# Kernel tuning notes

Hardware: AMD Instinct MI355X
Metric: run time of the kernel (lower is better)

## Reference

```python
import jax, jax.numpy as jnp
import numpy as np


def setup_inputs() -> dict:
    key = jax.random.key(0)
    k1, k2, k3 = jax.random.split(key, 3)
    B, N, F, U = 8, 2048, 128, 128
    A = jax.random.uniform(k1, (B, N, N), dtype=jnp.float32)   # dense nonneg adjacency
    X = jax.random.normal(k2, (B, N, F), dtype=jnp.float32)
    W = jax.random.normal(k3, (F, U), dtype=jnp.float32)
    bias = jnp.zeros((U,), dtype=jnp.float32)
    p = jnp.zeros((1,), dtype=jnp.float32)
    q = jnp.zeros((1,), dtype=jnp.float32)
    return {"A": A, "X": X, "W": W, "bias": bias, "p": p, "q": q}


def reference(A, X, W, bias, p, q):
    # learn_pqr path of MyGCN: A_ = D @ (A + q*I) @ D with D = diag(k^-0.25),
    # k = p + (1-p)*colsum(A). Diag matmuls expressed as broadcasted scaling (same math).
    B, N, _ = A.shape
    ps = jax.nn.sigmoid(p)          # shape (1,)
    qs = jax.nn.sigmoid(q)
    Dr = jnp.sum(A, axis=1)          # [B, N]  (K.sum axis=1)
    k_vec = ps + (1.0 - ps) * Dr     # [B, N]
    k_inv_root = jnp.sqrt(k_vec) ** -0.5   # k^{-0.25}
    k_clean = jnp.where(jnp.isinf(k_inv_root), 0.0, k_inv_root)  # [B, N]
    I = jnp.eye(N, dtype=A.dtype)
    AqI = A + qs[0] * I              # [B, N, N]
    A_ = k_clean[:, :, None] * AqI * k_clean[:, None, :]
    XW = jnp.einsum('bnf,fu->bnu', X, W)        # [B, N, U]
    A_XW = jnp.einsum('bnm,bmu->bnu', A_, XW)   # [B, N, U]
    out = A_XW + bias
    return jax.nn.relu(out)
```

## Files before the change

### kernel.cpp

```cpp
#include <hip/hip_runtime.h>
#include <stdint.h>

#define N 2048
#define F 128
#define UDIM 128

typedef __attribute__((ext_vector_type(8))) __bf16 bf16x8;
typedef __attribute__((ext_vector_type(8))) unsigned short us8;
typedef __attribute__((ext_vector_type(4))) float f32x4;

__device__ __forceinline__ unsigned short f2bf(float f) {
  union { float f; uint32_t u; } v; v.f = f;
  uint32_t u = v.u;
  return (unsigned short)((u + 0x7FFFu + ((u >> 16) & 1u)) >> 16);
}
__device__ __forceinline__ float bf2f(unsigned short u) {
  union { uint32_t u; float f; } v; v.u = ((uint32_t)u) << 16; return v.f;
}

__device__ __forceinline__ void async_load16(const void* g, void* l) {
  typedef const __attribute__((address_space(1))) uint32_t* gp_t;
  typedef __attribute__((address_space(3))) uint32_t* lp_t;
  __builtin_amdgcn_global_load_lds((gp_t)(uintptr_t)g, (lp_t)(uint32_t)(uintptr_t)l, 16, 0, 0);
}

__global__ __launch_bounds__(256)
void gcn_colsum(const float* __restrict__ A, const float* __restrict__ W,
                float* __restrict__ partial, unsigned short* __restrict__ WTb) {
  const int b = blockIdx.z;
  const int rc = blockIdx.y;
  const int j = blockIdx.x * 1024 + threadIdx.x * 4;
  const float* ap = A + (size_t)b * N * N + (size_t)rc * 32 * N + j;
  float s0 = 0.f, s1 = 0.f, s2 = 0.f, s3 = 0.f;
  #pragma unroll 4
  for (int rr = 0; rr < 32; ++rr) {
    float4 v = *(const float4*)(ap + (size_t)rr * N);
    s0 += v.x; s1 += v.y; s2 += v.z; s3 += v.w;
  }
  float4 s; s.x = s0; s.y = s1; s.z = s2; s.w = s3;
  *(float4*)&partial[((size_t)b * 64 + rc) * N + j] = s;

  if (blockIdx.y == 0 && blockIdx.z == 0) {
    #pragma unroll 4
    for (int it = 0; it < 32; ++it) {
      const int flat = it * 512 + blockIdx.x * 256 + threadIdx.x;
      const int k_ = flat >> 7;
      const int u = flat & 127;
      WTb[u * 128 + k_] = f2bf(W[flat]);
    }
  }
}

__global__ __launch_bounds__(256, 2)
void gcn_xwT(const float* __restrict__ X, const unsigned short* __restrict__ WTb,
             const float* __restrict__ partial, const float* __restrict__ pptr,
             float* __restrict__ kcl, unsigned short* __restrict__ YT) {
  __shared__ __align__(16) unsigned short Wl[128 * 128];
  __shared__ __align__(16) unsigned short Xl[32 * 128];
  __shared__ float red[8][33];
  __shared__ float kct[32];

  const int t = threadIdx.x;
  const int lane = t & 63;
  const int wid = t >> 6;
  const int b = blockIdx.x >> 6;
  const int i0 = (blockIdx.x & 63) << 5;

  #pragma unroll
  for (int rnd = 0; rnd < 8; ++rnd) {
    const int u = rnd * 16 + (t >> 4);
    const int c16 = (t & 15) ^ (u & 7);
    async_load16(WTb + u * 128 + c16 * 8, &Wl[rnd * 2048 + (t & ~63) * 8]);
  }
  {
    const int r = t >> 3;
    const float* xp = X + ((size_t)b * N + i0 + r) * F + (t & 7) * 8;
    #pragma unroll
    for (int h = 0; h < 2; ++h) {
      float4 v0 = *(const float4*)(xp + h * 64);
      float4 v1 = *(const float4*)(xp + h * 64 + 4);
      us8 w;
      w[0] = f2bf(v0.x); w[1] = f2bf(v0.y); w[2] = f2bf(v0.z); w[3] = f2bf(v0.w);
      w[4] = f2bf(v1.x); w[5] = f2bf(v1.y); w[6] = f2bf(v1.z); w[7] = f2bf(v1.w);
      const int slot = (t & 7) + h * 8;
      *(us8*)&Xl[r * 128 + ((slot ^ (r & 7)) * 8)] = w;
    }
  }
  {
    const int col = t & 31;
    const int grp = t >> 5;
    float s = 0.f;
    #pragma unroll
    for (int rr = 0; rr < 8; ++rr)
      s += partial[((size_t)b * 64 + grp * 8 + rr) * N + i0 + col];
    red[grp][col] = s;
  }
  __syncthreads();
  if (t < 32) {
    float s = 0.f;
    #pragma unroll
    for (int g = 0; g < 8; ++g) s += red[g][t];
    const float sp = 1.0f / (1.0f + __expf(-pptr[0]));
    const float k = sp + (1.0f - sp) * s;
    float rv = rsqrtf(sqrtf(k));
    if (isinf(rv)) rv = 0.f;
    kct[t] = rv;
    kcl[b * N + i0 + t] = rv;
  }
  __syncthreads();

  f32x4 acc[2][2];
  #pragma unroll
  for (int a = 0; a < 2; ++a)
    #pragma unroll
    for (int c = 0; c < 2; ++c) { f32x4 z = {0.f, 0.f, 0.f, 0.f}; acc[a][c] = z; }

  const int u0 = wid * 32;
  #pragma unroll
  for (int kc = 0; kc < 4; ++kc) {
    bf16x8 af[2], bfv[2];
    #pragma unroll
    for (int ut = 0; ut < 2; ++ut) {
      const int u = u0 + ut * 16 + (lane & 15);
      const int sl = ((kc * 4 + (lane >> 4)) ^ (u & 7)) * 8;
      af[ut] = *(const bf16x8*)&Wl[u * 128 + sl];
    }
    #pragma unroll
    for (int it = 0; it < 2; ++it) {
      const int rr = it * 16 + (lane & 15);
      const int sl = ((kc * 4 + (lane >> 4)) ^ (rr & 7)) * 8;
      bfv[it] = *(const bf16x8*)&Xl[rr * 128 + sl];
    }
    #pragma unroll
    for (int ut = 0; ut < 2; ++ut)
      #pragma unroll
      for (int it = 0; it < 2; ++it)
        acc[ut][it] = __builtin_amdgcn_mfma_f32_16x16x32_bf16(af[ut], bfv[it], acc[ut][it], 0, 0, 0);
  }

  #pragma unroll
  for (int ut = 0; ut < 2; ++ut) {
    #pragma unroll
    for (int it = 0; it < 2; ++it) {
      const int ic = it * 16 + (lane & 15);
      const float kv = kct[ic];
      #pragma unroll
      for (int rg = 0; rg < 4; ++rg) {
        const int u = u0 + ut * 16 + (lane >> 4) * 4 + rg;
        YT[(size_t)b * UDIM * N + (size_t)u * N + i0 + ic] = f2bf(acc[ut][it][rg] * kv);
      }
    }
  }
}

__global__ __launch_bounds__(256, 2)
void gcn_gemm(const float* __restrict__ A, const unsigned short* __restrict__ YT,
              const float* __restrict__ kcl, const float* __restrict__ bias,
              const float* __restrict__ qptr, float* __restrict__ out) {
  __shared__ __align__(16) unsigned short Abuf[3][32 * 64];
  __shared__ __align__(16) unsigned short Ybuf[3][128 * 64];

  const int t = threadIdx.x;
  const int lane = t & 63;
  const int wid = t >> 6;
  const int wr = wid >> 1;
  const int wc = wid & 1;

  const int bid = blockIdx.x;
  const int b = bid & 7;
  const int i0 = (bid >> 3) << 5;

  const float qs = 1.0f / (1.0f + __expf(-qptr[0]));

  const int r = t >> 3;
  const int c8 = t & 7;
  const float* Ap = A + (size_t)b * N * N + (size_t)(i0 + r) * N + c8 * 8;
  const unsigned short* YTb = YT + (size_t)b * UDIM * N;

  const int a_woff = r * 64 + ((c8 ^ (r & 7)) * 8);
  const int y_u = t >> 3;
  const int y_wavebase = (t & ~63) * 8;

  f32x4 acc[4];
  #pragma unroll
  for (int i = 0; i < 4; ++i) { f32x4 z = {0.f, 0.f, 0.f, 0.f}; acc[i] = z; }

  float4 ar0, ar1;

  auto issueA = [&](int kt) {
    ar0 = *(const float4*)(Ap + kt * 64);
    ar1 = *(const float4*)(Ap + kt * 64 + 4);
  };
  auto issueY = [&](int kt, int buf) {
    const int k0 = kt * 64;
    #pragma unroll
    for (int rnd = 0; rnd < 4; ++rnd) {
      const int u = rnd * 32 + y_u;
      const int c16 = (t & 7) ^ (u & 7);
      async_load16(YTb + (size_t)u * N + k0 + c16 * 8, &Ybuf[buf][rnd * 2048 + y_wavebase]);
    }
  };
  auto convertA = [&](int buf) {
    us8 w;
    w[0] = f2bf(ar0.x); w[1] = f2bf(ar0.y); w[2] = f2bf(ar0.z); w[3] = f2bf(ar0.w);
    w[4] = f2bf(ar1.x); w[5] = f2bf(ar1.y); w[6] = f2bf(ar1.z); w[7] = f2bf(ar1.w);
    *(us8*)&Abuf[buf][a_woff] = w;
  };
  auto compute = [&](int cur) {
    #pragma unroll
    for (int kk = 0; kk < 2; ++kk) {
      const int ar = 16 * wr + (lane & 15);
      const int as = ((kk * 4 + (lane >> 4)) ^ (ar & 7)) * 8;
      bf16x8 af = *(const bf16x8*)&Abuf[cur][ar * 64 + as];
      #pragma unroll
      for (int ut = 0; ut < 4; ++ut) {
        const int u = 64 * wc + ut * 16 + (lane & 15);
        const int bs = ((kk * 4 + (lane >> 4)) ^ (u & 7)) * 8;
        bf16x8 bfv = *(const bf16x8*)&Ybuf[cur][u * 64 + bs];
        acc[ut] = __builtin_amdgcn_mfma_f32_16x16x32_bf16(af, bfv, acc[ut], 0, 0, 0);
      }
    }
  };

#define STEP(KT, CUR, NXT, ISS)                                  \
  {                                                              \
    asm volatile("s_waitcnt vmcnt(4)" ::: "memory");             \
    convertA(NXT);                                               \
    asm volatile("s_waitcnt lgkmcnt(0)" ::: "memory");           \
    __builtin_amdgcn_s_barrier();                                \
    __builtin_amdgcn_sched_barrier(0);                           \
    issueA((KT) + 2);                                            \
    __builtin_amdgcn_sched_barrier(0);                           \
    issueY((KT) + 2, (ISS));                                     \
    __builtin_amdgcn_sched_barrier(0);                           \
    compute(CUR);                                                \
  }

  issueA(0);
  __builtin_amdgcn_sched_barrier(0);
  issueY(0, 0);
  __builtin_amdgcn_sched_barrier(0);
  asm volatile("s_waitcnt vmcnt(4)" ::: "memory");
  convertA(0);
  __builtin_amdgcn_sched_barrier(0);
  issueA(1);
  __builtin_amdgcn_sched_barrier(0);
  issueY(1, 1);
  __builtin_amdgcn_sched_barrier(0);

  #pragma unroll 1
  for (int kt0 = 0; kt0 < 30; kt0 += 3) {
    STEP(kt0,     0, 1, 2);
    STEP(kt0 + 1, 1, 2, 0);
    STEP(kt0 + 2, 2, 0, 1);
  }
#undef STEP

  asm volatile("s_waitcnt vmcnt(4)" ::: "memory");
  convertA(1);
  asm volatile("s_waitcnt lgkmcnt(0)" ::: "memory");
  __builtin_amdgcn_s_barrier();
  __builtin_amdgcn_sched_barrier(0);
  compute(0);
  asm volatile("s_waitcnt vmcnt(0)" ::: "memory");
  __builtin_amdgcn_s_barrier();
  __builtin_amdgcn_sched_barrier(0);
  compute(1);

  const int irow = i0 + 16 * wr + (lane >> 4) * 4;
  #pragma unroll
  for (int ut = 0; ut < 4; ++ut) {
    const int u = 64 * wc + ut * 16 + (lane & 15);
    const float bv = bias[u];
    #pragma unroll
    for (int rg = 0; rg < 4; ++rg) {
      const int i = irow + rg;
      const float yv = bf2f(YTb[(size_t)u * N + i]);
      const float kv = kcl[b * N + i];
      float vv = kv * (acc[ut][rg] + qs * yv) + bv;
      out[((size_t)b * N + i) * UDIM + u] = vv > 0.f ? vv : 0.f;
    }
  }
}

extern "C" void kernel_launch(void* const* d_in, const int* in_sizes, int n_in,
                              void* d_out, int out_size, void* d_ws, size_t ws_size,
                              hipStream_t stream) {
  (void)in_sizes; (void)n_in; (void)out_size; (void)ws_size;
  const float* A    = (const float*)d_in[0];
  const float* X    = (const float*)d_in[1];
  const float* W    = (const float*)d_in[2];
  const float* bias = (const float*)d_in[3];
  const float* p    = (const float*)d_in[4];
  const float* q    = (const float*)d_in[5];
  float* out = (float*)d_out;

  char* ws = (char*)d_ws;
  float* partial      = (float*)ws;
  float* kcl          = (float*)(ws + 4194304);
  unsigned short* WTb = (unsigned short*)(ws + 4194304 + 65536);
  unsigned short* YT  = (unsigned short*)(ws + 4292608);

  gcn_colsum<<<dim3(2, 64, 8), dim3(256), 0, stream>>>(A, W, partial, WTb);
  gcn_xwT<<<dim3(512), dim3(256), 0, stream>>>(X, WTb, partial, p, kcl, YT);
  gcn_gemm<<<dim3(512), dim3(256), 0, stream>>>(A, YT, kcl, bias, q, out);
}
```

Measured before the change: 62.15 us.

## Merge colsum with XW GEMM, add scale pass, deepen main GEMM pipeline

```diff
diff --git a/kernel.cpp b/kernel.cpp
--- a/kernel.cpp
+++ b/kernel.cpp
@@ -17,6 +17,11 @@
 __device__ __forceinline__ float bf2f(unsigned short u) {
   union { uint32_t u; float f; } v; v.u = ((uint32_t)u) << 16; return v.f;
 }
+__device__ __forceinline__ uint32_t cvtpk(float lo, float hi) {
+  uint32_t r;
+  asm("v_cvt_pk_bf16_f32 %0, %1, %2" : "=v"(r) : "v"(lo), "v"(hi));
+  return r;
+}
 
 __device__ __forceinline__ void async_load16(const void* g, void* l) {
   typedef const __attribute__((address_space(1))) uint32_t* gp_t;
@@ -24,53 +29,53 @@
   __builtin_amdgcn_global_load_lds((gp_t)(uintptr_t)g, (lp_t)(uint32_t)(uintptr_t)l, 16, 0, 0);
 }
 
-__global__ __launch_bounds__(256)
-void gcn_colsum(const float* __restrict__ A, const float* __restrict__ W,
-                float* __restrict__ partial, unsigned short* __restrict__ WTb) {
-  const int b = blockIdx.z;
-  const int rc = blockIdx.y;
-  const int j = blockIdx.x * 1024 + threadIdx.x * 4;
-  const float* ap = A + (size_t)b * N * N + (size_t)rc * 32 * N + j;
-  float s0 = 0.f, s1 = 0.f, s2 = 0.f, s3 = 0.f;
-  #pragma unroll 4
-  for (int rr = 0; rr < 32; ++rr) {
-    float4 v = *(const float4*)(ap + (size_t)rr * N);
-    s0 += v.x; s1 += v.y; s2 += v.z; s3 += v.w;
-  }
-  float4 s; s.x = s0; s.y = s1; s.z = s2; s.w = s3;
-  *(float4*)&partial[((size_t)b * 64 + rc) * N + j] = s;
-
-  if (blockIdx.y == 0 && blockIdx.z == 0) {
-    #pragma unroll 4
-    for (int it = 0; it < 32; ++it) {
-      const int flat = it * 512 + blockIdx.x * 256 + threadIdx.x;
-      const int k_ = flat >> 7;
-      const int u = flat & 127;
-      WTb[u * 128 + k_] = f2bf(W[flat]);
-    }
-  }
-}
-
-__global__ __launch_bounds__(256, 2)
-void gcn_xwT(const float* __restrict__ X, const unsigned short* __restrict__ WTb,
-             const float* __restrict__ partial, const float* __restrict__ pptr,
-             float* __restrict__ kcl, unsigned short* __restrict__ YT) {
+__global__ __launch_bounds__(256, 4)
+void gcn_pass1(const float* __restrict__ A, const float* __restrict__ X,
+               const float* __restrict__ W, float* __restrict__ partial,
+               unsigned short* __restrict__ Z) {
   __shared__ __align__(16) unsigned short Wl[128 * 128];
   __shared__ __align__(16) unsigned short Xl[32 * 128];
-  __shared__ float red[8][33];
-  __shared__ float kct[32];
-
+
+  const int bid = blockIdx.x;
   const int t = threadIdx.x;
+
+  if (bid < 1024) {
+    const int b = bid >> 7;
+    const int rc = (bid >> 1) & 63;
+    const int j = (bid & 1) * 1024 + t * 4;
+    const float* ap = A + (size_t)b * N * N + (size_t)rc * 32 * N + j;
+    float s0 = 0.f, s1 = 0.f, s2 = 0.f, s3 = 0.f;
+    #pragma unroll 4
+    for (int rr = 0; rr < 32; ++rr) {
+      float4 v = *(const float4*)(ap + (size_t)rr * N);
+      s0 += v.x; s1 += v.y; s2 += v.z; s3 += v.w;
+    }
+    float4 s; s.x = s0; s.y = s1; s.z = s2; s.w = s3;
+    *(float4*)&partial[((size_t)b * 64 + rc) * N + j] = s;
+    return;
+  }
+
+  const int zid = bid - 1024;
   const int lane = t & 63;
   const int wid = t >> 6;
-  const int b = blockIdx.x >> 6;
-  const int i0 = (blockIdx.x & 63) << 5;
-
-  #pragma unroll
-  for (int rnd = 0; rnd < 8; ++rnd) {
-    const int u = rnd * 16 + (t >> 4);
-    const int c16 = (t & 15) ^ (u & 7);
-    async_load16(WTb + u * 128 + c16 * 8, &Wl[rnd * 2048 + (t & ~63) * 8]);
+  const int b = zid >> 6;
+  const int i0 = (zid & 63) << 5;
+
+  {
+    const int u = t & 127;
+    const int khalf = t >> 7;
+    #pragma unroll
+    for (int g = 0; g < 8; ++g) {
+      const int k0 = khalf * 64 + g * 8;
+      float v[8];
+      #pragma unroll
+      for (int e = 0; e < 8; ++e) v[e] = W[(size_t)(k0 + e) * 128 + u];
+      uint4 w;
+      w.x = cvtpk(v[0], v[1]); w.y = cvtpk(v[2], v[3]);
+      w.z = cvtpk(v[4], v[5]); w.w = cvtpk(v[6], v[7]);
+      const int slot = khalf * 8 + g;
+      *(uint4*)&Wl[u * 128 + ((slot ^ (u & 7)) * 8)] = w;
+    }
   }
   {
     const int r = t >> 3;
@@ -79,77 +84,101 @@
     for (int h = 0; h < 2; ++h) {
       float4 v0 = *(const float4*)(xp + h * 64);
       float4 v1 = *(const float4*)(xp + h * 64 + 4);
-      us8 w;
-      w[0] = f2bf(v0.x); w[1] = f2bf(v0.y); w[2] = f2bf(v0.z); w[3] = f2bf(v0.w);
-      w[4] = f2bf(v1.x); w[5] = f2bf(v1.y); w[6] = f2bf(v1.z); w[7] = f2bf(v1.w);
+      uint4 w;
+      w.x = cvtpk(v0.x, v0.y); w.y = cvtpk(v0.z, v0.w);
+      w.z = cvtpk(v1.x, v1.y); w.w = cvtpk(v1.z, v1.w);
       const int slot = (t & 7) + h * 8;
-      *(us8*)&Xl[r * 128 + ((slot ^ (r & 7)) * 8)] = w;
-    }
-  }
+      *(uint4*)&Xl[r * 128 + ((slot ^ (r & 7)) * 8)] = w;
+    }
+  }
+  __syncthreads();
+
+  f32x4 acc[2][2];
+  #pragma unroll
+  for (int a = 0; a < 2; ++a)
+    #pragma unroll
+    for (int c = 0; c < 2; ++c) { f32x4 z = {0.f, 0.f, 0.f, 0.f}; acc[a][c] = z; }
+
+  const int u0 = wid * 32;
+  #pragma unroll
+  for (int kc = 0; kc < 4; ++kc) {
+    bf16x8 af[2], bfv[2];
+    #pragma unroll
+    for (int ut = 0; ut < 2; ++ut) {
+      const int u = u0 + ut * 16 + (lane & 15);
+      const int sl = ((kc * 4 + (lane >> 4)) ^ (u & 7)) * 8;
+      af[ut] = *(const bf16x8*)&Wl[u * 128 + sl];
+    }
+    #pragma unroll
+    for (int it = 0; it < 2; ++it) {
+      const int rr = it * 16 + (lane & 15);
+      const int sl = ((kc * 4 + (lane >> 4)) ^ (rr & 7)) * 8;
+      bfv[it] = *(const bf16x8*)&Xl[rr * 128 + sl];
+    }
+    #pragma unroll
+    for (int ut = 0; ut < 2; ++ut)
+      #pragma unroll
+      for (int it = 0; it < 2; ++it)
+        acc[ut][it] = __builtin_amdgcn_mfma_f32_16x16x32_bf16(af[ut], bfv[it], acc[ut][it], 0, 0, 0);
+  }
+
+  #pragma unroll
+  for (int ut = 0; ut < 2; ++ut)
+    #pragma unroll
+    for (int it = 0; it < 2; ++it) {
+      const int ic = i0 + it * 16 + (lane & 15);
+      #pragma unroll
+      for (int rg = 0; rg < 4; ++rg) {
+        const int u = u0 + ut * 16 + (lane >> 4) * 4 + rg;
+        Z[((size_t)b * UDIM + u) * N + ic] = f2bf(acc[ut][it][rg]);
+      }
+    }
+}
+
+__global__ __launch_bounds__(256, 4)
+void gcn_scale(const float* __restrict__ partial, const float* __restrict__ pptr,
+               const unsigned short* __restrict__ Z, float* __restrict__ kcl,
+               unsigned short* __restrict__ YT) {
+  __shared__ float red[2][128];
+  __shared__ float kct[128];
+  const int t = threadIdx.x;
+  const int b = blockIdx.x >> 4;
+  const int ic = (blockIdx.x & 15) * 128;
+
   {
-    const int col = t & 31;
-    const int grp = t >> 5;
+    const int i = ic + (t & 127);
+    const int half = t >> 7;
     float s = 0.f;
-    #pragma unroll
-    for (int rr = 0; rr < 8; ++rr)
-      s += partial[((size_t)b * 64 + grp * 8 + rr) * N + i0 + col];
-    red[grp][col] = s;
+    #pragma unroll 8
+    for (int rc = half * 32; rc < half * 32 + 32; ++rc)
+      s += partial[((size_t)b * 64 + rc) * N + i];
+    red[half][t & 127] = s;
   }
   __syncthreads();
-  if (t < 32) {
-    float s = 0.f;
-    #pragma unroll
-    for (int g = 0; g < 8; ++g) s += red[g][t];
+  if (t < 128) {
+    const float s = red[0][t] + red[1][t];
     const float sp = 1.0f / (1.0f + __expf(-pptr[0]));
     const float k = sp + (1.0f - sp) * s;
     float rv = rsqrtf(sqrtf(k));
     if (isinf(rv)) rv = 0.f;
     kct[t] = rv;
-    kcl[b * N + i0 + t] = rv;
+    kcl[b * N + ic + t] = rv;
   }
   __syncthreads();
 
-  f32x4 acc[2][2];
-  #pragma unroll
-  for (int a = 0; a < 2; ++a)
-    #pragma unroll
-    for (int c = 0; c < 2; ++c) { f32x4 z = {0.f, 0.f, 0.f, 0.f}; acc[a][c] = z; }
-
-  const int u0 = wid * 32;
-  #pragma unroll
-  for (int kc = 0; kc < 4; ++kc) {
-    bf16x8 af[2], bfv[2];
-    #pragma unroll
-    for (int ut = 0; ut < 2; ++ut) {
-      const int u = u0 + ut * 16 + (lane & 15);
-      const int sl = ((kc * 4 + (lane >> 4)) ^ (u & 7)) * 8;
-      af[ut] = *(const bf16x8*)&Wl[u * 128 + sl];
-    }
-    #pragma unroll
-    for (int it = 0; it < 2; ++it) {
-      const int rr = it * 16 + (lane & 15);
-      const int sl = ((kc * 4 + (lane >> 4)) ^ (rr & 7)) * 8;
-      bfv[it] = *(const bf16x8*)&Xl[rr * 128 + sl];
-    }
-    #pragma unroll
-    for (int ut = 0; ut < 2; ++ut)
-      #pragma unroll
-      for (int it = 0; it < 2; ++it)
-        acc[ut][it] = __builtin_amdgcn_mfma_f32_16x16x32_bf16(af[ut], bfv[it], acc[ut][it], 0, 0, 0);
-  }
-
-  #pragma unroll
-  for (int ut = 0; ut < 2; ++ut) {
-    #pragma unroll
-    for (int it = 0; it < 2; ++it) {
-      const int ic = it * 16 + (lane & 15);
-      const float kv = kct[ic];
-      #pragma unroll
-      for (int rg = 0; rg < 4; ++rg) {
-        const int u = u0 + ut * 16 + (lane >> 4) * 4 + rg;
-        YT[(size_t)b * UDIM * N + (size_t)u * N + i0 + ic] = f2bf(acc[ut][it][rg] * kv);
-      }
-    }
+  const int i8 = (t & 15) * 8;
+  #pragma unroll
+  for (int it = 0; it < 8; ++it) {
+    const int u = it * 16 + (t >> 4);
+    const size_t off = ((size_t)b * UDIM + u) * N + ic + i8;
+    us8 z = *(const us8*)&Z[off];
+    float y[8];
+    #pragma unroll
+    for (int e = 0; e < 8; ++e) y[e] = bf2f(z[e]) * kct[i8 + e];
+    uint4 w;
+    w.x = cvtpk(y[0], y[1]); w.y = cvtpk(y[2], y[3]);
+    w.z = cvtpk(y[4], y[5]); w.w = cvtpk(y[6], y[7]);
+    *(uint4*)&YT[off] = w;
   }
 }
 
@@ -157,8 +186,8 @@
 void gcn_gemm(const float* __restrict__ A, const unsigned short* __restrict__ YT,
               const float* __restrict__ kcl, const float* __restrict__ bias,
               const float* __restrict__ qptr, float* __restrict__ out) {
-  __shared__ __align__(16) unsigned short Abuf[3][32 * 64];
-  __shared__ __align__(16) unsigned short Ybuf[3][128 * 64];
+  __shared__ __align__(16) unsigned short Abuf[4 * 32 * 64];
+  __shared__ __align__(16) unsigned short Ybuf[4 * 128 * 64];
 
   const int t = threadIdx.x;
   const int lane = t & 63;
@@ -185,87 +214,84 @@
   #pragma unroll
   for (int i = 0; i < 4; ++i) { f32x4 z = {0.f, 0.f, 0.f, 0.f}; acc[i] = z; }
 
-  float4 ar0, ar1;
-
-  auto issueA = [&](int kt) {
-    ar0 = *(const float4*)(Ap + kt * 64);
-    ar1 = *(const float4*)(Ap + kt * 64 + 4);
-  };
+  float4 a0A, a1A, a0B, a1B;
+
   auto issueY = [&](int kt, int buf) {
     const int k0 = kt * 64;
     #pragma unroll
     for (int rnd = 0; rnd < 4; ++rnd) {
       const int u = rnd * 32 + y_u;
       const int c16 = (t & 7) ^ (u & 7);
-      async_load16(YTb + (size_t)u * N + k0 + c16 * 8, &Ybuf[buf][rnd * 2048 + y_wavebase]);
-    }
-  };
-  auto convertA = [&](int buf) {
-    us8 w;
-    w[0] = f2bf(ar0.x); w[1] = f2bf(ar0.y); w[2] = f2bf(ar0.z); w[3] = f2bf(ar0.w);
-    w[4] = f2bf(ar1.x); w[5] = f2bf(ar1.y); w[6] = f2bf(ar1.z); w[7] = f2bf(ar1.w);
-    *(us8*)&Abuf[buf][a_woff] = w;
+      async_load16(YTb + (size_t)u * N + k0 + c16 * 8, &Ybuf[buf * 8192 + rnd * 2048 + y_wavebase]);
+    }
   };
   auto compute = [&](int cur) {
+    const unsigned short* Ac = Abuf + cur * 2048;
+    const unsigned short* Yc = Ybuf + cur * 8192;
     #pragma unroll
     for (int kk = 0; kk < 2; ++kk) {
       const int ar = 16 * wr + (lane & 15);
       const int as = ((kk * 4 + (lane >> 4)) ^ (ar & 7)) * 8;
-      bf16x8 af = *(const bf16x8*)&Abuf[cur][ar * 64 + as];
+      bf16x8 af = *(const bf16x8*)&Ac[ar * 64 + as];
       #pragma unroll
       for (int ut = 0; ut < 4; ++ut) {
         const int u = 64 * wc + ut * 16 + (lane & 15);
         const int bs = ((kk * 4 + (lane >> 4)) ^ (u & 7)) * 8;
-        bf16x8 bfv = *(const bf16x8*)&Ybuf[cur][u * 64 + bs];
+        bf16x8 bfv = *(const bf16x8*)&Yc[u * 64 + bs];
         acc[ut] = __builtin_amdgcn_mfma_f32_16x16x32_bf16(af, bfv, acc[ut], 0, 0, 0);
       }
     }
   };
 
-#define STEP(KT, CUR, NXT, ISS)                                  \
-  {                                                              \
-    asm volatile("s_waitcnt vmcnt(4)" ::: "memory");             \
-    convertA(NXT);                                               \
-    asm volatile("s_waitcnt lgkmcnt(0)" ::: "memory");           \
-    __builtin_amdgcn_s_barrier();                                \
-    __builtin_amdgcn_sched_barrier(0);                           \
-    issueA((KT) + 2);                                            \
-    __builtin_amdgcn_sched_barrier(0);                           \
-    issueY((KT) + 2, (ISS));                                     \
-    __builtin_amdgcn_sched_barrier(0);                           \
-    compute(CUR);                                                \
-  }
-
-  issueA(0);
-  __builtin_amdgcn_sched_barrier(0);
-  issueY(0, 0);
-  __builtin_amdgcn_sched_barrier(0);
+#define SB __builtin_amdgcn_sched_barrier(0)
+#define ISSUE_A(KT, R0, R1) { R0 = *(const float4*)(Ap + (KT) * 64); R1 = *(const float4*)(Ap + (KT) * 64 + 4); }
+#define CVT_A(BUF, R0, R1) { \
+    uint4 w; w.x = cvtpk(R0.x, R0.y); w.y = cvtpk(R0.z, R0.w); \
+    w.z = cvtpk(R1.x, R1.y); w.w = cvtpk(R1.z, R1.w); \
+    *(uint4*)&Abuf[(BUF) * 2048 + a_woff] = w; }
+
+  ISSUE_A(0, a0A, a1A); SB;
+  ISSUE_A(1, a0B, a1B); SB;
+  issueY(0, 0); SB;
+  asm volatile("s_waitcnt vmcnt(6)" ::: "memory");
+  CVT_A(0, a0A, a1A); SB;
+  ISSUE_A(2, a0A, a1A); SB;
+  issueY(1, 1); SB;
+  asm volatile("s_waitcnt vmcnt(10)" ::: "memory");
+  CVT_A(1, a0B, a1B); SB;
+  ISSUE_A(3, a0B, a1B); SB;
+  issueY(2, 2); SB;
+
+#define GSTEP(KT, VM, R0, R1, DO_A, DO_Y)                          \
+  {                                                                \
+    asm volatile("s_waitcnt vmcnt(" #VM ")" ::: "memory");         \
+    CVT_A(((KT) + 2) & 3, R0, R1);                                 \
+    asm volatile("s_waitcnt lgkmcnt(0)" ::: "memory");             \
+    __builtin_amdgcn_s_barrier(); SB;                              \
+    if (DO_A) { ISSUE_A((KT) + 4, R0, R1); } SB;                   \
+    if (DO_Y) { issueY((KT) + 3, ((KT) + 3) & 3); } SB;            \
+    __builtin_amdgcn_s_setprio(1);                                 \
+    compute((KT) & 3);                                             \
+    __builtin_amdgcn_s_setprio(0); SB;                             \
+  }
+
+  #pragma unroll 1
+  for (int kt = 0; kt < 28; kt += 2) {
+    GSTEP(kt, 10, a0A, a1A, true, true);
+    GSTEP(kt + 1, 10, a0B, a1B, true, true);
+  }
+  GSTEP(28, 10, a0A, a1A, false, true);
+  GSTEP(29, 8, a0B, a1B, false, false);
   asm volatile("s_waitcnt vmcnt(4)" ::: "memory");
-  convertA(0);
-  __builtin_amdgcn_sched_barrier(0);
-  issueA(1);
-  __builtin_amdgcn_sched_barrier(0);
-  issueY(1, 1);
-  __builtin_amdgcn_sched_barrier(0);
-
-  #pragma unroll 1
-  for (int kt0 = 0; kt0 < 30; kt0 += 3) {
-    STEP(kt0,     0, 1, 2);
-    STEP(kt0 + 1, 1, 2, 0);
-    STEP(kt0 + 2, 2, 0, 1);
-  }
-#undef STEP
-
-  asm volatile("s_waitcnt vmcnt(4)" ::: "memory");
-  convertA(1);
-  asm volatile("s_waitcnt lgkmcnt(0)" ::: "memory");
-  __builtin_amdgcn_s_barrier();
-  __builtin_amdgcn_sched_barrier(0);
-  compute(0);
+  __builtin_amdgcn_s_barrier(); SB;
+  compute(2);
   asm volatile("s_waitcnt vmcnt(0)" ::: "memory");
-  __builtin_amdgcn_s_barrier();
-  __builtin_amdgcn_sched_barrier(0);
-  compute(1);
+  __builtin_amdgcn_s_barrier(); SB;
+  compute(3);
+#undef GSTEP
+#undef CVT_A
+#undef ISSUE_A
+#undef SB
 
   const int irow = i0 + 16 * wr + (lane >> 4) * 4;
   #pragma unroll
@@ -298,10 +324,10 @@
   char* ws = (char*)d_ws;
   float* partial      = (float*)ws;
   float* kcl          = (float*)(ws + 4194304);
-  unsigned short* WTb = (unsigned short*)(ws + 4194304 + 65536);
-  unsigned short* YT  = (unsigned short*)(ws + 4292608);
-
-  gcn_colsum<<<dim3(2, 64, 8), dim3(256), 0, stream>>>(A, W, partial, WTb);
-  gcn_xwT<<<dim3(512), dim3(256), 0, stream>>>(X, WTb, partial, p, kcl, YT);
+  unsigned short* Zb  = (unsigned short*)(ws + 4259840);
+  unsigned short* YT  = (unsigned short*)(ws + 8454144);
+
+  gcn_pass1<<<dim3(1536), dim3(256), 0, stream>>>(A, X, W, partial, Zb);
+  gcn_scale<<<dim3(128), dim3(256), 0, stream>>>(partial, p, Zb, kcl, YT);
   gcn_gemm<<<dim3(512), dim3(256), 0, stream>>>(A, YT, kcl, bias, q, out);
 }
```

Measured after the change: 58.86 us. 1.06x faster.
